# Kernel tuning notes

Hardware: AMD Instinct MI355X
Metric: run time of the kernel (lower is better)

Reference implementation:

```python
import jax, jax.numpy as jnp
import numpy as np

B, S, D_IN, D_QK, D_V = 4, 4096, 1024, 64, 64

def setup_inputs() -> dict:
    key = jax.random.key(0)
    ks = jax.random.split(key, 8)
    sd = 1.0 / np.sqrt(D_IN)
    return {
        "X": jax.random.normal(ks[0], (B, S, D_IN), dtype=jnp.float32),
        "mask": jnp.ones((B, S, 1), dtype=jnp.float32),
        "Wq": jax.random.uniform(ks[1], (D_IN, D_QK), jnp.float32, -sd, sd),
        "bq": jax.random.uniform(ks[2], (D_QK,), jnp.float32, -sd, sd),
        "Wk": jax.random.uniform(ks[3], (D_IN, D_QK), jnp.float32, -sd, sd),
        "bk": jax.random.uniform(ks[4], (D_QK,), jnp.float32, -sd, sd),
        "Wv": jax.random.uniform(ks[5], (D_IN, D_V), jnp.float32, -sd, sd),
        "bv": jax.random.uniform(ks[6], (D_V,), jnp.float32, -sd, sd),
    }

def reference(X, mask, Wq, bq, Wk, bk, Wv, bv):
    # ReLU-activated projections (no head split, no 1/sqrt(d) scaling)
    q = jax.nn.relu(jnp.einsum('bsd,df->bsf', X, Wq) + bq)   # [B,S,D_QK]
    k = jax.nn.relu(jnp.einsum('bsd,df->bsf', X, Wk) + bk)   # [B,S,D_QK]
    v = jax.nn.relu(jnp.einsum('bsd,df->bsf', X, Wv) + bv)   # [B,S,D_V]
    scores = jax.nn.softmax(jnp.einsum('bqf,bkf->bqk', q, k), axis=-1)  # [B,S,S]
    return jnp.einsum('bqk,bkf->bqf', scores, v) * mask       # mask applied AFTER AV
```

## Files before the change

kernel.cpp:

```cpp
#include <hip/hip_runtime.h>


typedef short s16x8 __attribute__((ext_vector_type(8)));
typedef float fx4   __attribute__((ext_vector_type(4)));
typedef unsigned short u16x4 __attribute__((ext_vector_type(4)));

#define LOG2E 1.4426950408889634f

__device__ __forceinline__ unsigned short f2bf(float x) {
    unsigned int u = __float_as_uint(x);
    u += 0x7FFFu + ((u >> 16) & 1u);
    return (unsigned short)(u >> 16);
}
__device__ __forceinline__ float bf2f(unsigned short b) {
    return __uint_as_float(((unsigned int)b) << 16);
}

__global__ __launch_bounds__(256) void prep_w_kernel(
    const float* __restrict__ Wq, const float* __restrict__ Wk, const float* __restrict__ Wv,
    unsigned short* __restrict__ wt_hi, unsigned short* __restrict__ wt_lo)
{
    __shared__ __align__(16) unsigned short sh[64][72];
    __shared__ __align__(16) unsigned short sl[64][72];

    const int y  = blockIdx.x;
    const int kt = blockIdx.y;
    const float* W = (y == 0) ? Wq : (y == 1) ? Wk : Wv;
    const int t  = threadIdx.x;

    const int kl = t >> 2;
    const int c0 = (t & 3) * 16;
    const float* src = W + (size_t)(kt * 64 + kl) * 64 + c0;
    #pragma unroll
    for (int j = 0; j < 4; j++) {
        fx4 v = *(const fx4*)(src + j * 4);
        #pragma unroll
        for (int i = 0; i < 4; i++) {
            float x = v[i];
            unsigned short h = f2bf(x);
            unsigned short l = f2bf(x - bf2f(h));
            sh[c0 + j * 4 + i][kl] = h;
            sl[c0 + j * 4 + i][kl] = l;
        }
    }
    __syncthreads();

    const int c  = t >> 2;
    const int k0 = (t & 3) * 16;
    size_t o = (size_t)(y * 64 + c) * 1024 + kt * 64 + k0;
    *(s16x8*)(wt_hi + o)     = *(const s16x8*)&sh[c][k0];
    *(s16x8*)(wt_hi + o + 8) = *(const s16x8*)&sh[c][k0 + 8];
    *(s16x8*)(wt_lo + o)     = *(const s16x8*)&sl[c][k0];
    *(s16x8*)(wt_lo + o + 8) = *(const s16x8*)&sl[c][k0 + 8];
}

__global__ __launch_bounds__(512, 4) void proj_kernel(
    const float* __restrict__ X,
    const unsigned short* __restrict__ wt_hi, const unsigned short* __restrict__ wt_lo,
    const float* __restrict__ bq, const float* __restrict__ bk, const float* __restrict__ bv,
    unsigned short* __restrict__ q_hi, unsigned short* __restrict__ q_lo,
    unsigned short* __restrict__ k_bf, unsigned short* __restrict__ vt_g)
{
    __shared__ __align__(16) unsigned short a_buf[2][64][72];
    __shared__ __align__(16) unsigned short b_hi[64][72];
    __shared__ __align__(16) unsigned short b_lo[64][72];

    const int tid  = threadIdx.x;
    const int lane = tid & 63;
    const int w    = tid >> 6;
    const int quad = lane >> 4;
    const int l15  = lane & 15;
    const int rs   = w & 3;
    const int ch   = w >> 2;

    const int f   = blockIdx.x;
    const int xcd = f & 7;
    const int jj  = f >> 3;
    const int y   = jj % 3;
    const int m0  = ((jj / 3) * 8 + xcd) * 64;

    fx4 acc[2];
    acc[0] = (fx4){0.f, 0.f, 0.f, 0.f};
    acc[1] = (fx4){0.f, 0.f, 0.f, 0.f};

    const int xrow = tid >> 4;
    const int xoff = (tid & 15) * 4;
    const int wrow = tid >> 3;
    const int woff = (tid & 7) * 8;

    const float* xb0 = X + (size_t)(m0 + xrow) * 1024 + xoff;
    const float* xb1 = X + (size_t)(m0 + xrow + 32) * 1024 + xoff;
    const size_t wb  = (size_t)(y * 64 + wrow) * 1024 + woff;

    fx4   xr[4][2];
    s16x8 wrh[2], wrl[2];
    #pragma unroll
    for (int d = 0; d < 4; d++) {
        xr[d][0] = *(const fx4*)(xb0 + d * 64);
        xr[d][1] = *(const fx4*)(xb1 + d * 64);
    }
    #pragma unroll
    for (int d = 0; d < 2; d++) {
        wrh[d] = *(const s16x8*)(wt_hi + wb + d * 64);
        wrl[d] = *(const s16x8*)(wt_lo + wb + d * 64);
    }

    #pragma unroll 4
    for (int kc = 0; kc < 16; kc++) {
        if (kc) __syncthreads();
        #pragma unroll
        for (int i = 0; i < 2; i++) {
            fx4 xv = xr[kc & 3][i];
            unsigned short h0 = f2bf(xv.x), h1 = f2bf(xv.y), h2 = f2bf(xv.z), h3 = f2bf(xv.w);
            unsigned short l0 = f2bf(xv.x - bf2f(h0)), l1 = f2bf(xv.y - bf2f(h1));
            unsigned short l2 = f2bf(xv.z - bf2f(h2)), l3 = f2bf(xv.w - bf2f(h3));
            *(u16x4*)&a_buf[0][xrow + i * 32][xoff] = (u16x4){h0, h1, h2, h3};
            *(u16x4*)&a_buf[1][xrow + i * 32][xoff] = (u16x4){l0, l1, l2, l3};
        }
        *(s16x8*)&b_hi[wrow][woff] = wrh[kc & 1];
        *(s16x8*)&b_lo[wrow][woff] = wrl[kc & 1];
        __syncthreads();

        if (kc < 12) {
            xr[kc & 3][0] = *(const fx4*)(xb0 + (kc + 4) * 64);
            xr[kc & 3][1] = *(const fx4*)(xb1 + (kc + 4) * 64);
        }
        if (kc < 14) {
            wrh[kc & 1] = *(const s16x8*)(wt_hi + wb + (kc + 2) * 64);
            wrl[kc & 1] = *(const s16x8*)(wt_lo + wb + (kc + 2) * 64);
        }

        s16x8 ah[2], al[2];
        #pragma unroll
        for (int ks = 0; ks < 2; ks++) {
            int r = rs * 16 + l15;
            ah[ks] = *(const s16x8*)&a_buf[0][r][ks * 32 + quad * 8];
            al[ks] = *(const s16x8*)&a_buf[1][r][ks * 32 + quad * 8];
        }
        #pragma unroll
        for (int nt = 0; nt < 2; nt++) {
            #pragma unroll
            for (int ks = 0; ks < 2; ks++) {
                s16x8 bh = *(const s16x8*)&b_hi[ch * 32 + nt * 16 + l15][ks * 32 + quad * 8];
                s16x8 bl = *(const s16x8*)&b_lo[ch * 32 + nt * 16 + l15][ks * 32 + quad * 8];
                acc[nt] = __builtin_amdgcn_mfma_f32_16x16x32_bf16(ah[ks], bh, acc[nt], 0, 0, 0);
                acc[nt] = __builtin_amdgcn_mfma_f32_16x16x32_bf16(ah[ks], bl, acc[nt], 0, 0, 0);
                acc[nt] = __builtin_amdgcn_mfma_f32_16x16x32_bf16(al[ks], bh, acc[nt], 0, 0, 0);
            }
        }
    }
    __syncthreads();

    const float* bias = (y == 0) ? bq : (y == 1) ? bk : bv;
    const int b   = m0 >> 12;
    const int s0b = m0 & 4095;
    unsigned short* vtr = &a_buf[0][0][0];

    #pragma unroll
    for (int nt = 0; nt < 2; nt++) {
        int col = ch * 32 + nt * 16 + l15;
        float bb = bias[col];
        int rloc = rs * 16 + quad * 4;
        #pragma unroll
        for (int r = 0; r < 4; r++) {
            float v = acc[nt][r] + bb;
            v = fmaxf(v, 0.f);
            size_t grow = (size_t)(m0 + rloc + r);
            if (y == 0) {
                unsigned short h = f2bf(v);
                unsigned short l = f2bf(v - bf2f(h));
                q_hi[grow * 64 + col] = h;
                q_lo[grow * 64 + col] = l;
            } else if (y == 1) {
                k_bf[grow * 64 + col] = f2bf(v);
            } else {
                vtr[col * 72 + rloc + r] = f2bf(v);
            }
        }
    }
    if (y == 2) {
        __syncthreads();
        int row = tid >> 3;
        int off = (tid & 7) * 8;
        s16x8 vv = *(const s16x8*)&vtr[row * 72 + off];
        *(s16x8*)(vt_g + (size_t)(b * 64 + row) * 4096 + s0b + off) = vv;
    }
}

__global__ __launch_bounds__(256, 6) void attn_kernel(
    const unsigned short* __restrict__ q_hi, const unsigned short* __restrict__ q_lo,
    const unsigned short* __restrict__ k_bf, const unsigned short* __restrict__ vt_g,
    unsigned short* __restrict__ pOb, float* __restrict__ pL)
{
    __shared__ __align__(16) unsigned short kt[64][72];
    __shared__ __align__(16) unsigned short vt[64][72];
    __shared__ __align__(16) unsigned short pt[4][16][40];

    const int tid  = threadIdx.x;
    const int lane = tid & 63;
    const int w    = tid >> 6;
    const int quad = lane >> 4;
    const int l15  = lane & 15;
    const int ck   = blockIdx.y;
    const int b    = blockIdx.z;
    const int q0   = blockIdx.x * 64;

    const size_t qoff = ((size_t)b * 4096 + q0 + w * 16 + l15) * 64 + quad * 8;
    s16x8 qh0 = *(const s16x8*)(q_hi + qoff);
    s16x8 qh1 = *(const s16x8*)(q_hi + qoff + 32);
    s16x8 ql0 = *(const s16x8*)(q_lo + qoff);
    s16x8 ql1 = *(const s16x8*)(q_lo + qoff + 32);

    fx4 accO[4];
    #pragma unroll
    for (int nt = 0; nt < 4; nt++) accO[nt] = (fx4){0.f, 0.f, 0.f, 0.f};
    float lsum[4] = {0.f, 0.f, 0.f, 0.f};

    const unsigned short* kgb = k_bf + (size_t)b * 4096 * 64;
    const unsigned short* vgb = vt_g + (size_t)b * 64 * 4096;

    const int srow = tid >> 3;
    const int soff = (tid & 7) * 8;

    for (int it = ck * 8; it < ck * 8 + 8; it++) {
        const unsigned short* kg = kgb + (size_t)it * 4096;
        #pragma unroll
        for (int i = 0; i < 2; i++) {
            int row = srow + i * 32;
            *(s16x8*)&kt[row][soff] = *(const s16x8*)(kg + (size_t)row * 64 + soff);
            *(s16x8*)&vt[row][soff] = *(const s16x8*)(vgb + (size_t)row * 4096 + it * 64 + soff);
        }
        __syncthreads();

        #pragma unroll
        for (int kh = 0; kh < 2; kh++) {
            #pragma unroll
            for (int nt2 = 0; nt2 < 2; nt2++) {
                int key = kh * 32 + nt2 * 16 + l15;
                s16x8 k0 = *(const s16x8*)&kt[key][quad * 8];
                s16x8 k1 = *(const s16x8*)&kt[key][32 + quad * 8];
                fx4 sc = (fx4){0.f, 0.f, 0.f, 0.f};
                sc = __builtin_amdgcn_mfma_f32_16x16x32_bf16(qh0, k0, sc, 0, 0, 0);
                sc = __builtin_amdgcn_mfma_f32_16x16x32_bf16(ql0, k0, sc, 0, 0, 0);
                sc = __builtin_amdgcn_mfma_f32_16x16x32_bf16(qh1, k1, sc, 0, 0, 0);
                sc = __builtin_amdgcn_mfma_f32_16x16x32_bf16(ql1, k1, sc, 0, 0, 0);
                #pragma unroll
                for (int r = 0; r < 4; r++) {
                    float p = __builtin_amdgcn_exp2f(sc[r] * LOG2E);
                    unsigned short pb = f2bf(p);
                    lsum[r] += bf2f(pb);
                    pt[w][quad * 4 + r][nt2 * 16 + l15] = pb;
                }
            }
            s16x8 pa = *(const s16x8*)&pt[w][l15][quad * 8];
            #pragma unroll
            for (int nt = 0; nt < 4; nt++) {
                s16x8 vf = *(const s16x8*)&vt[nt * 16 + l15][kh * 32 + quad * 8];
                accO[nt] = __builtin_amdgcn_mfma_f32_16x16x32_bf16(pa, vf, accO[nt], 0, 0, 0);
            }
        }
        __syncthreads();
    }

    #pragma unroll
    for (int r = 0; r < 4; r++) {
        float v = lsum[r];
        #pragma unroll
        for (int o = 1; o < 16; o <<= 1) v += __shfl_xor(v, o);
        lsum[r] = v;
    }
    #pragma unroll
    for (int r = 0; r < 4; r++) {
        int qrow = q0 + w * 16 + quad * 4 + r;
        size_t grow = (size_t)b * 4096 + qrow;
        #pragma unroll
        for (int nt = 0; nt < 4; nt++)
            pOb[((size_t)ck * 16384 + grow) * 64 + nt * 16 + l15] = f2bf(accO[nt][r]);
        if (l15 == 0)
            pL[(size_t)ck * 16384 + grow] = lsum[r];
    }
}

__global__ __launch_bounds__(256) void combine_kernel(
    const unsigned short* __restrict__ pOb, const float* __restrict__ pL,
    const float* __restrict__ mask, float* __restrict__ out)
{
    int idx = blockIdx.x * 256 + threadIdx.x;
    int q  = idx >> 4;
    int dg = idx & 15;
    fx4 s = (fx4){0.f, 0.f, 0.f, 0.f};
    float l = 0.f;
    #pragma unroll
    for (int c = 0; c < 8; c++) {
        u16x4 h = *(const u16x4*)(pOb + ((size_t)c * 16384 + q) * 64 + dg * 4);
        s.x += bf2f(h.x);
        s.y += bf2f(h.y);
        s.z += bf2f(h.z);
        s.w += bf2f(h.w);
        l += pL[(size_t)c * 16384 + q];
    }
    float scale = mask[q] / l;
    *(fx4*)(out + (size_t)q * 64 + dg * 4) = s * scale;
}

extern "C" void kernel_launch(void* const* d_in, const int* in_sizes, int n_in,
                              void* d_out, int out_size, void* d_ws, size_t ws_size,
                              hipStream_t stream)
{
    const float* X    = (const float*)d_in[0];
    const float* mask = (const float*)d_in[1];
    const float* Wq   = (const float*)d_in[2];
    const float* bq   = (const float*)d_in[3];
    const float* Wk   = (const float*)d_in[4];
    const float* bk   = (const float*)d_in[5];
    const float* Wv   = (const float*)d_in[6];
    const float* bv   = (const float*)d_in[7];
    float* out = (float*)d_out;

    char* ws = (char*)d_ws;
    unsigned short* q_hi  = (unsigned short*)(ws);
    unsigned short* q_lo  = (unsigned short*)(ws + (size_t)(2u << 20));
    unsigned short* k_bf  = (unsigned short*)(ws + (size_t)(4u << 20));
    unsigned short* vt_g  = (unsigned short*)(ws + (size_t)(6u << 20));
    unsigned short* wt_hi = (unsigned short*)(ws + (size_t)(8u << 20));
    unsigned short* wt_lo = (unsigned short*)(ws + (size_t)(8u << 20) + 393216);
    unsigned short* pOb   = (unsigned short*)(ws + (size_t)(9u << 20));
    float*          pL    = (float*)(ws + (size_t)(25u << 20));

    hipLaunchKernelGGL(prep_w_kernel, dim3(3, 16), dim3(256), 0, stream,
                       Wq, Wk, Wv, wt_hi, wt_lo);
    hipLaunchKernelGGL(proj_kernel, dim3(768), dim3(512), 0, stream,
                       X, wt_hi, wt_lo, bq, bk, bv, q_hi, q_lo, k_bf, vt_g);
    hipLaunchKernelGGL(attn_kernel, dim3(64, 8, 4), dim3(256), 0, stream,
                       q_hi, q_lo, k_bf, vt_g, pOb, pL);
    hipLaunchKernelGGL(combine_kernel, dim3(1024), dim3(256), 0, stream,
                       pOb, pL, mask, out);
}
```

Measured before the change: 175.2 us.

## Restructure projection GEMM to read X directly into MFMA registers

The projection kernel now uses 256 threads, with each wave owning 16 rows and all 64 output columns. X is loaded straight from global memory into registers in MFMA operand layout and split into hi/lo bf16 in registers, so the X tile no longer goes through LDS. Only the weights are staged in LDS, in 128-wide K chunks, which halves the number of barriers per block. The cost is uncoalesced strided X loads per lane and fewer threads per block, plus changed occupancy.

Result: slower. 180.2 us (+2.8%).

```diff
diff --git a/kernel.cpp b/kernel.cpp
--- a/kernel.cpp
+++ b/kernel.cpp
@@ -54,24 +54,20 @@
     *(s16x8*)(wt_lo + o + 8) = *(const s16x8*)&sl[c][k0 + 8];
 }
 
-__global__ __launch_bounds__(512, 4) void proj_kernel(
+__global__ __launch_bounds__(256, 3) void proj_kernel(
     const float* __restrict__ X,
     const unsigned short* __restrict__ wt_hi, const unsigned short* __restrict__ wt_lo,
     const float* __restrict__ bq, const float* __restrict__ bk, const float* __restrict__ bv,
     unsigned short* __restrict__ q_hi, unsigned short* __restrict__ q_lo,
     unsigned short* __restrict__ k_bf, unsigned short* __restrict__ vt_g)
 {
-    __shared__ __align__(16) unsigned short a_buf[2][64][72];
-    __shared__ __align__(16) unsigned short b_hi[64][72];
-    __shared__ __align__(16) unsigned short b_lo[64][72];
+    __shared__ __align__(16) unsigned short wls[2][64][136];
 
     const int tid  = threadIdx.x;
     const int lane = tid & 63;
     const int w    = tid >> 6;
     const int quad = lane >> 4;
     const int l15  = lane & 15;
-    const int rs   = w & 3;
-    const int ch   = w >> 2;
 
     const int f   = blockIdx.x;
     const int xcd = f & 7;
@@ -79,73 +75,87 @@
     const int y   = jj % 3;
     const int m0  = ((jj / 3) * 8 + xcd) * 64;
 
-    fx4 acc[2];
-    acc[0] = (fx4){0.f, 0.f, 0.f, 0.f};
-    acc[1] = (fx4){0.f, 0.f, 0.f, 0.f};
-
-    const int xrow = tid >> 4;
-    const int xoff = (tid & 15) * 4;
-    const int wrow = tid >> 3;
-    const int woff = (tid & 7) * 8;
-
-    const float* xb0 = X + (size_t)(m0 + xrow) * 1024 + xoff;
-    const float* xb1 = X + (size_t)(m0 + xrow + 32) * 1024 + xoff;
-    const size_t wb  = (size_t)(y * 64 + wrow) * 1024 + woff;
-
-    fx4   xr[4][2];
-    s16x8 wrh[2], wrl[2];
-    #pragma unroll
-    for (int d = 0; d < 4; d++) {
-        xr[d][0] = *(const fx4*)(xb0 + d * 64);
-        xr[d][1] = *(const fx4*)(xb1 + d * 64);
-    }
-    #pragma unroll
-    for (int d = 0; d < 2; d++) {
-        wrh[d] = *(const s16x8*)(wt_hi + wb + d * 64);
-        wrl[d] = *(const s16x8*)(wt_lo + wb + d * 64);
-    }
-
-    #pragma unroll 4
-    for (int kc = 0; kc < 16; kc++) {
-        if (kc) __syncthreads();
-        #pragma unroll
-        for (int i = 0; i < 2; i++) {
-            fx4 xv = xr[kc & 3][i];
-            unsigned short h0 = f2bf(xv.x), h1 = f2bf(xv.y), h2 = f2bf(xv.z), h3 = f2bf(xv.w);
-            unsigned short l0 = f2bf(xv.x - bf2f(h0)), l1 = f2bf(xv.y - bf2f(h1));
-            unsigned short l2 = f2bf(xv.z - bf2f(h2)), l3 = f2bf(xv.w - bf2f(h3));
-            *(u16x4*)&a_buf[0][xrow + i * 32][xoff] = (u16x4){h0, h1, h2, h3};
-            *(u16x4*)&a_buf[1][xrow + i * 32][xoff] = (u16x4){l0, l1, l2, l3};
-        }
-        *(s16x8*)&b_hi[wrow][woff] = wrh[kc & 1];
-        *(s16x8*)&b_lo[wrow][woff] = wrl[kc & 1];
+    const int row = m0 + w * 16 + l15;
+    const float* xbase = X + (size_t)row * 1024;
+
+    const int wcol = tid >> 2;
+    const int wk0  = (tid & 3) * 32;
+    const size_t wgb = (size_t)(y * 64 + wcol) * 1024 + wk0;
+
+    s16x8 wrh[4], wrl[4];
+    #pragma unroll
+    for (int i = 0; i < 4; i++) {
+        wrh[i] = *(const s16x8*)(wt_hi + wgb + i * 8);
+        wrl[i] = *(const s16x8*)(wt_lo + wgb + i * 8);
+    }
+    fx4 xc[2][2];
+    #pragma unroll
+    for (int ks = 0; ks < 2; ks++) {
+        xc[ks][0] = *(const fx4*)(xbase + ks * 32 + quad * 8);
+        xc[ks][1] = *(const fx4*)(xbase + ks * 32 + quad * 8 + 4);
+    }
+
+    fx4 acc[4];
+    #pragma unroll
+    for (int nt = 0; nt < 4; nt++) acc[nt] = (fx4){0.f, 0.f, 0.f, 0.f};
+
+    for (int ch = 0; ch < 8; ch++) {
+        if (ch) __syncthreads();
+        #pragma unroll
+        for (int i = 0; i < 4; i++) {
+            *(s16x8*)&wls[0][wcol][wk0 + i * 8] = wrh[i];
+            *(s16x8*)&wls[1][wcol][wk0 + i * 8] = wrl[i];
+        }
         __syncthreads();
-
-        if (kc < 12) {
-            xr[kc & 3][0] = *(const fx4*)(xb0 + (kc + 4) * 64);
-            xr[kc & 3][1] = *(const fx4*)(xb1 + (kc + 4) * 64);
-        }
-        if (kc < 14) {
-            wrh[kc & 1] = *(const s16x8*)(wt_hi + wb + (kc + 2) * 64);
-            wrl[kc & 1] = *(const s16x8*)(wt_lo + wb + (kc + 2) * 64);
-        }
-
-        s16x8 ah[2], al[2];
-        #pragma unroll
-        for (int ks = 0; ks < 2; ks++) {
-            int r = rs * 16 + l15;
-            ah[ks] = *(const s16x8*)&a_buf[0][r][ks * 32 + quad * 8];
-            al[ks] = *(const s16x8*)&a_buf[1][r][ks * 32 + quad * 8];
-        }
-        #pragma unroll
-        for (int nt = 0; nt < 2; nt++) {
+        if (ch < 7) {
+            #pragma unroll
+            for (int i = 0; i < 4; i++) {
+                wrh[i] = *(const s16x8*)(wt_hi + wgb + (ch + 1) * 128 + i * 8);
+                wrl[i] = *(const s16x8*)(wt_lo + wgb + (ch + 1) * 128 + i * 8);
+            }
+        }
+
+        #pragma unroll
+        for (int kk = 0; kk < 2; kk++) {
+            const int kc = ch * 2 + kk;
+            fx4 xn[2][2];
+            if (kc < 15) {
+                #pragma unroll
+                for (int ks = 0; ks < 2; ks++) {
+                    xn[ks][0] = *(const fx4*)(xbase + (kc + 1) * 64 + ks * 32 + quad * 8);
+                    xn[ks][1] = *(const fx4*)(xbase + (kc + 1) * 64 + ks * 32 + quad * 8 + 4);
+                }
+            }
+            s16x8 ah[2], al[2];
             #pragma unroll
             for (int ks = 0; ks < 2; ks++) {
-                s16x8 bh = *(const s16x8*)&b_hi[ch * 32 + nt * 16 + l15][ks * 32 + quad * 8];
-                s16x8 bl = *(const s16x8*)&b_lo[ch * 32 + nt * 16 + l15][ks * 32 + quad * 8];
-                acc[nt] = __builtin_amdgcn_mfma_f32_16x16x32_bf16(ah[ks], bh, acc[nt], 0, 0, 0);
-                acc[nt] = __builtin_amdgcn_mfma_f32_16x16x32_bf16(ah[ks], bl, acc[nt], 0, 0, 0);
-                acc[nt] = __builtin_amdgcn_mfma_f32_16x16x32_bf16(al[ks], bh, acc[nt], 0, 0, 0);
+                #pragma unroll
+                for (int j = 0; j < 2; j++) {
+                    fx4 v = xc[ks][j];
+                    #pragma unroll
+                    for (int i = 0; i < 4; i++) {
+                        unsigned short h = f2bf(v[i]);
+                        ah[ks][j * 4 + i] = (short)h;
+                        al[ks][j * 4 + i] = (short)f2bf(v[i] - bf2f(h));
+                    }
+                }
+            }
+            #pragma unroll
+            for (int nt = 0; nt < 4; nt++) {
+                #pragma unroll
+                for (int ks = 0; ks < 2; ks++) {
+                    const int ko = kk * 64 + ks * 32 + quad * 8;
+                    s16x8 bh = *(const s16x8*)&wls[0][nt * 16 + l15][ko];
+                    s16x8 bl = *(const s16x8*)&wls[1][nt * 16 + l15][ko];
+                    acc[nt] = __builtin_amdgcn_mfma_f32_16x16x32_bf16(ah[ks], bh, acc[nt], 0, 0, 0);
+                    acc[nt] = __builtin_amdgcn_mfma_f32_16x16x32_bf16(ah[ks], bl, acc[nt], 0, 0, 0);
+                    acc[nt] = __builtin_amdgcn_mfma_f32_16x16x32_bf16(al[ks], bh, acc[nt], 0, 0, 0);
+                }
+            }
+            #pragma unroll
+            for (int ks = 0; ks < 2; ks++) {
+                xc[ks][0] = xn[ks][0];
+                xc[ks][1] = xn[ks][1];
             }
         }
     }
@@ -154,13 +164,13 @@
     const float* bias = (y == 0) ? bq : (y == 1) ? bk : bv;
     const int b   = m0 >> 12;
     const int s0b = m0 & 4095;
-    unsigned short* vtr = &a_buf[0][0][0];
-
-    #pragma unroll
-    for (int nt = 0; nt < 2; nt++) {
-        int col = ch * 32 + nt * 16 + l15;
+    unsigned short* vtr = &wls[0][0][0];
+
+    #pragma unroll
+    for (int nt = 0; nt < 4; nt++) {
+        int col = nt * 16 + l15;
         float bb = bias[col];
-        int rloc = rs * 16 + quad * 4;
+        int rloc = w * 16 + quad * 4;
         #pragma unroll
         for (int r = 0; r < 4; r++) {
             float v = acc[nt][r] + bb;
@@ -180,10 +190,12 @@
     }
     if (y == 2) {
         __syncthreads();
-        int row = tid >> 3;
-        int off = (tid & 7) * 8;
-        s16x8 vv = *(const s16x8*)&vtr[row * 72 + off];
-        *(s16x8*)(vt_g + (size_t)(b * 64 + row) * 4096 + s0b + off) = vv;
+        int rowd = tid >> 2;
+        int off  = (tid & 3) * 16;
+        s16x8 v0 = *(const s16x8*)&vtr[rowd * 72 + off];
+        s16x8 v1 = *(const s16x8*)&vtr[rowd * 72 + off + 8];
+        *(s16x8*)(vt_g + (size_t)(b * 64 + rowd) * 4096 + s0b + off)     = v0;
+        *(s16x8*)(vt_g + (size_t)(b * 64 + rowd) * 4096 + s0b + off + 8) = v1;
     }
 }
 
@@ -329,7 +341,7 @@
 
     hipLaunchKernelGGL(prep_w_kernel, dim3(3, 16), dim3(256), 0, stream,
                        Wq, Wk, Wv, wt_hi, wt_lo);
-    hipLaunchKernelGGL(proj_kernel, dim3(768), dim3(512), 0, stream,
+    hipLaunchKernelGGL(proj_kernel, dim3(768), dim3(256), 0, stream,
                        X, wt_hi, wt_lo, bq, bk, bv, q_hi, q_lo, k_bf, vt_g);
     hipLaunchKernelGGL(attn_kernel, dim3(64, 8, 4), dim3(256), 0, stream,
                        q_hi, q_lo, k_bf, vt_g, pOb, pL);
```
